# Kernel optimization log

Hardware: AMD Instinct MI355X
Metric: run time of the kernel (lower is better)

Reference implementation:

```python
import jax, jax.numpy as jnp
import numpy as np

N_SRC = 200000
N_DST = 50000
N_EDGES = 800000
IN_FEATS = 128
OUT_FEATS = 64


def setup_inputs() -> dict:
    key = jax.random.key(0)
    k1, k2, k3, k4 = jax.random.split(key, 4)
    x = jax.random.normal(k1, (N_SRC, IN_FEATS), dtype=jnp.float32)
    edge_src = jax.random.randint(k2, (N_EDGES,), 0, N_SRC, dtype=jnp.int64)
    edge_dst = jax.random.randint(k3, (N_EDGES,), 0, N_DST, dtype=jnp.int64)
    W = jax.random.normal(k4, (IN_FEATS, OUT_FEATS), dtype=jnp.float32) / np.sqrt(IN_FEATS)
    b = jnp.zeros((OUT_FEATS,), dtype=jnp.float32)
    return {"x": x, "edge_src": edge_src, "edge_dst": edge_dst, "W": W, "b": b, "n_dst": N_DST}


def reference(x, edge_src, edge_dst, W, b, n_dst):
    # DGL SAGEConv, aggregator_type='gcn'.
    # lin_before_mp = in_feats > out_feats (128 > 64) -> project before aggregation.
    h_src = x @ W                      # [n_src, out]
    h_dst = h_src[:n_dst]              # dst nodes are the first n_dst src nodes
    # sparse gather + segment reduce (SpMM): sum of projected neighbor feats per dst
    msgs = h_src[edge_src]             # [n_edges, out]
    neigh_sum = jax.ops.segment_sum(msgs, edge_dst, num_segments=n_dst)
    deg = jax.ops.segment_sum(jnp.ones_like(edge_dst, dtype=h_src.dtype),
                              edge_dst, num_segments=n_dst)  # in-degree per dst
    h = (neigh_sum + h_dst) / (deg + 1.0)[:, None]
    return h + b
```

## Files before the change

### kernel.cpp

```cpp
#include <hip/hip_runtime.h>
#include <hip/hip_bf16.h>

#define IN_F   128
#define OUT_F  64
#define NG 768
#define NB 256
#define CAP 64

typedef __attribute__((ext_vector_type(8))) short short8;
typedef __attribute__((ext_vector_type(4))) float floatx4;

__device__ inline unsigned short f32_to_bf16_rne(float f) {
    unsigned int u = __float_as_uint(f);
    unsigned int r = (u + 0x7FFFu + ((u >> 16) & 1u)) >> 16;
    return (unsigned short)r;
}
__device__ inline float bf16_to_f32(unsigned short u) {
    return __uint_as_float((unsigned int)u << 16);
}
__device__ inline unsigned int cvt_pk_bf16(float lo, float hi) {
    unsigned int r;
    asm volatile("v_cvt_pk_bf16_f32 %0, %1, %2" : "=v"(r) : "v"(lo), "v"(hi));
    return r;
}

__global__ __launch_bounds__(256) void prep_w(const float* __restrict__ W,
                                              unsigned short* __restrict__ Wtg) {
    const int o = blockIdx.x * 256 + threadIdx.x;
    #pragma unroll
    for (int m = 0; m < 4; ++m) {
        const int idx = o + m * 2048;
        const int f = idx >> 9, r = idx & 511, l = r >> 3, j = r & 7;
        const int t = f >> 2, s = f & 3;
        const int k = 32 * s + 8 * (l >> 4) + j;
        const int c = 16 * t + (l & 15);
        Wtg[idx] = f32_to_bf16_rne(W[k * 64 + c]);
    }
}

__global__ __launch_bounds__(256, 1) void gemm_bin(const float* __restrict__ x,
                                                   const unsigned short* __restrict__ Wtg,
                                                   unsigned short* __restrict__ h,
                                                   int nTiles,
                                                   const int* __restrict__ esrc,
                                                   const int* __restrict__ edst,
                                                   int* __restrict__ cnt,
                                                   int* __restrict__ elist,
                                                   int n_edges) {
    const int tid = threadIdx.x;

    if (blockIdx.x >= NG) {
        const int stride = NB * 256;
        for (int e = (blockIdx.x - NG) * 256 + tid; e < n_edges; e += stride) {
            const int d = edst[e];
            const int slot = atomicAdd(&cnt[d], 1);
            if (slot < CAP) elist[(size_t)d * CAP + slot] = esrc[e];
        }
        return;
    }

    const int lane = tid & 63;
    const int wave = tid >> 6;
    const int lrow = lane & 15;
    const int lkg  = lane >> 4;

    short8 bf[4][4];
    #pragma unroll
    for (int t = 0; t < 4; ++t)
        #pragma unroll
        for (int s = 0; s < 4; ++s)
            bf[t][s] = *reinterpret_cast<const short8*>(&Wtg[((t * 4 + s) * 64 + lane) * 8]);

    for (int tile = blockIdx.x; tile < nTiles; tile += NG) {
        const float* base = x + (size_t)tile * 64 * IN_F
                              + (size_t)(16 * wave + lrow) * IN_F + 8 * lkg;
        float4 x0 = *reinterpret_cast<const float4*>(base);
        float4 x1 = *reinterpret_cast<const float4*>(base + 4);
        float4 x2 = *reinterpret_cast<const float4*>(base + 32);
        float4 x3 = *reinterpret_cast<const float4*>(base + 36);
        float4 x4 = *reinterpret_cast<const float4*>(base + 64);
        float4 x5 = *reinterpret_cast<const float4*>(base + 68);
        float4 x6 = *reinterpret_cast<const float4*>(base + 96);
        float4 x7 = *reinterpret_cast<const float4*>(base + 100);

        short8 a0, a1, a2, a3;
        {
            union { unsigned int u[4]; short8 v; } cv;
            cv.u[0] = cvt_pk_bf16(x0.x, x0.y); cv.u[1] = cvt_pk_bf16(x0.z, x0.w);
            cv.u[2] = cvt_pk_bf16(x1.x, x1.y); cv.u[3] = cvt_pk_bf16(x1.z, x1.w);
            a0 = cv.v;
            cv.u[0] = cvt_pk_bf16(x2.x, x2.y); cv.u[1] = cvt_pk_bf16(x2.z, x2.w);
            cv.u[2] = cvt_pk_bf16(x3.x, x3.y); cv.u[3] = cvt_pk_bf16(x3.z, x3.w);
            a1 = cv.v;
            cv.u[0] = cvt_pk_bf16(x4.x, x4.y); cv.u[1] = cvt_pk_bf16(x4.z, x4.w);
            cv.u[2] = cvt_pk_bf16(x5.x, x5.y); cv.u[3] = cvt_pk_bf16(x5.z, x5.w);
            a2 = cv.v;
            cv.u[0] = cvt_pk_bf16(x6.x, x6.y); cv.u[1] = cvt_pk_bf16(x6.z, x6.w);
            cv.u[2] = cvt_pk_bf16(x7.x, x7.y); cv.u[3] = cvt_pk_bf16(x7.z, x7.w);
            a3 = cv.v;
        }

        floatx4 acc[4];
        #pragma unroll
        for (int t = 0; t < 4; ++t) acc[t] = (floatx4){0.f, 0.f, 0.f, 0.f};
        #pragma unroll
        for (int t = 0; t < 4; ++t) {
            acc[t] = __builtin_amdgcn_mfma_f32_16x16x32_bf16(a0, bf[t][0], acc[t], 0, 0, 0);
            acc[t] = __builtin_amdgcn_mfma_f32_16x16x32_bf16(a1, bf[t][1], acc[t], 0, 0, 0);
            acc[t] = __builtin_amdgcn_mfma_f32_16x16x32_bf16(a2, bf[t][2], acc[t], 0, 0, 0);
            acc[t] = __builtin_amdgcn_mfma_f32_16x16x32_bf16(a3, bf[t][3], acc[t], 0, 0, 0);
        }

        unsigned short* hb = h + ((size_t)tile * 64 + 16 * wave) * OUT_F;
        #pragma unroll
        for (int t = 0; t < 4; ++t)
            #pragma unroll
            for (int r = 0; r < 4; ++r)
                hb[(size_t)(4 * lkg + r) * OUT_F + 16 * t + lrow] =
                    f32_to_bf16_rne(acc[t][r]);
    }
}

__global__ __launch_bounds__(256) void gather_finalize(const unsigned short* __restrict__ h,
                                                       const int* __restrict__ cnt,
                                                       const int* __restrict__ elist,
                                                       const float* __restrict__ b,
                                                       float* __restrict__ out,
                                                       int n_dst) {
    const int lane = threadIdx.x & 63;
    const int d = blockIdx.x * 4 + (threadIdx.x >> 6);
    if (d >= n_dst) return;

    const int eq = lane >> 4;
    const int p  = lane & 15;

    const int cnt_d = cnt[d];
    const int m = min(cnt_d, CAP);
    const size_t ebase = (size_t)d * CAP;

    float4 acc = {0.f, 0.f, 0.f, 0.f};

    for (int base = 0; base < m; base += 64) {
        const int lim = min(64, m - base);
        const int sidx = (base + lane < m) ? elist[ebase + base + lane] : 0;
        for (int j = 0; j < lim; j += 4) {
            const int myj = j + eq;
            const bool valid = myj < lim;
            const int s = __shfl(sidx, valid ? myj : 0);
            const ushort4 v = *reinterpret_cast<const ushort4*>(&h[(size_t)s * OUT_F + 4 * p]);
            const float w = valid ? 1.0f : 0.0f;
            acc.x += w * bf16_to_f32(v.x);
            acc.y += w * bf16_to_f32(v.y);
            acc.z += w * bf16_to_f32(v.z);
            acc.w += w * bf16_to_f32(v.w);
        }
    }

    acc.x += __shfl_xor(acc.x, 32); acc.y += __shfl_xor(acc.y, 32);
    acc.z += __shfl_xor(acc.z, 32); acc.w += __shfl_xor(acc.w, 32);
    acc.x += __shfl_xor(acc.x, 16); acc.y += __shfl_xor(acc.y, 16);
    acc.z += __shfl_xor(acc.z, 16); acc.w += __shfl_xor(acc.w, 16);

    if (lane < 16) {
        const ushort4 hd = *reinterpret_cast<const ushort4*>(&h[(size_t)d * OUT_F + 4 * p]);
        const float4 bb = *reinterpret_cast<const float4*>(&b[4 * p]);
        const float inv = 1.0f / ((float)cnt_d + 1.0f);
        float4 o;
        o.x = (acc.x + bf16_to_f32(hd.x)) * inv + bb.x;
        o.y = (acc.y + bf16_to_f32(hd.y)) * inv + bb.y;
        o.z = (acc.z + bf16_to_f32(hd.z)) * inv + bb.z;
        o.w = (acc.w + bf16_to_f32(hd.w)) * inv + bb.w;
        *reinterpret_cast<float4*>(&out[(size_t)d * OUT_F + 4 * p]) = o;
    }
}

static inline size_t align256(size_t v) { return (v + 255) & ~(size_t)255; }

extern "C" void kernel_launch(void* const* d_in, const int* in_sizes, int n_in,
                              void* d_out, int out_size, void* d_ws, size_t ws_size,
                              hipStream_t stream) {
    const float* x    = (const float*)d_in[0];
    const int*   esrc = (const int*)d_in[1];
    const int*   edst = (const int*)d_in[2];
    const float* W    = (const float*)d_in[3];
    const float* b    = (const float*)d_in[4];

    const int n_rows  = in_sizes[0] / IN_F;
    const int n_edges = in_sizes[1];
    const int n_dst   = out_size / OUT_F;
    float* out = (float*)d_out;

    const size_t hBytes  = (size_t)n_rows * OUT_F * sizeof(unsigned short);
    const size_t cntOff  = align256(hBytes);
    const size_t elOff   = align256(cntOff + (size_t)n_dst * 4);
    const size_t wtOff   = align256(elOff + (size_t)n_dst * CAP * 4);
    const size_t needed  = wtOff + (size_t)IN_F * OUT_F * sizeof(unsigned short);

    unsigned short* h = (unsigned short*)d_ws;

    if (ws_size >= needed) {
        int* cnt             = (int*)((char*)d_ws + cntOff);
        int* elist           = (int*)((char*)d_ws + elOff);
        unsigned short* Wtg  = (unsigned short*)((char*)d_ws + wtOff);

        hipMemsetAsync(cnt, 0, (size_t)n_dst * 4, stream);

        prep_w<<<8, 256, 0, stream>>>(W, Wtg);

        const int nTiles = n_rows / 64;
        gemm_bin<<<NG + NB, 256, 0, stream>>>(x, Wtg, h, nTiles,
                                              esrc, edst, cnt, elist, n_edges);

        const int gBlocks = (n_dst + 3) / 4;
        gather_finalize<<<gBlocks, 256, 0, stream>>>(h, cnt, elist, b, out, n_dst);
    } else {
        hipMemsetAsync(out, 0, (size_t)out_size * sizeof(float), stream);
    }
}
```

Before: 95.94 us.

## Split edge binning into XCD-partitioned kernel with 16-bit dst indices

Edge binning moves out of the fused GEMM kernel into a separate kernel. Each block reads its XCD id from a hardware register and only handles destinations in that XCD's range, so atomics on cnt stay within one XCD's L2. A new prep kernel packs edge_dst into 16-bit values to cut the bytes each XCD rescans, and every XCD pulls edge chunks through its own atomic cursor. In exchange, each XCD now reads the whole dst array, there are extra kernel launches, and the GEMM no longer overlaps with binning. The 16-bit packing only holds while n_dst is below 65536.

```diff
diff --git a/kernel.cpp b/kernel.cpp
--- a/kernel.cpp
+++ b/kernel.cpp
@@ -3,12 +3,14 @@
 
 #define IN_F   128
 #define OUT_F  64
-#define NG 768
-#define NB 256
-#define CAP 64
+#define CAP    64
+#define NG     1024
+#define NBIN   2048
+#define CHUNK  2048
 
 typedef __attribute__((ext_vector_type(8))) short short8;
 typedef __attribute__((ext_vector_type(4))) float floatx4;
+typedef __attribute__((ext_vector_type(8))) unsigned short ushort8;
 
 __device__ inline unsigned short f32_to_bf16_rne(float f) {
     unsigned int u = __float_as_uint(f);
@@ -24,41 +26,81 @@
     return r;
 }
 
-__global__ __launch_bounds__(256) void prep_w(const float* __restrict__ W,
-                                              unsigned short* __restrict__ Wtg) {
-    const int o = blockIdx.x * 256 + threadIdx.x;
-    #pragma unroll
-    for (int m = 0; m < 4; ++m) {
-        const int idx = o + m * 2048;
-        const int f = idx >> 9, r = idx & 511, l = r >> 3, j = r & 7;
-        const int t = f >> 2, s = f & 3;
-        const int k = 32 * s + 8 * (l >> 4) + j;
-        const int c = 16 * t + (l & 15);
-        Wtg[idx] = f32_to_bf16_rne(W[k * 64 + c]);
-    }
-}
-
-__global__ __launch_bounds__(256, 1) void gemm_bin(const float* __restrict__ x,
-                                                   const unsigned short* __restrict__ Wtg,
-                                                   unsigned short* __restrict__ h,
-                                                   int nTiles,
-                                                   const int* __restrict__ esrc,
-                                                   const int* __restrict__ edst,
-                                                   int* __restrict__ cnt,
-                                                   int* __restrict__ elist,
-                                                   int n_edges) {
+__global__ __launch_bounds__(256) void prep(const float* __restrict__ W,
+                                            unsigned short* __restrict__ Wtg,
+                                            const int* __restrict__ edst,
+                                            unsigned short* __restrict__ edst16,
+                                            int n_edges) {
     const int tid = threadIdx.x;
-
-    if (blockIdx.x >= NG) {
-        const int stride = NB * 256;
-        for (int e = (blockIdx.x - NG) * 256 + tid; e < n_edges; e += stride) {
-            const int d = edst[e];
-            const int slot = atomicAdd(&cnt[d], 1);
-            if (slot < CAP) elist[(size_t)d * CAP + slot] = esrc[e];
+    if (blockIdx.x < 8) {
+        const int o = blockIdx.x * 256 + tid;
+        #pragma unroll
+        for (int m = 0; m < 4; ++m) {
+            const int idx = o + m * 2048;
+            const int f = idx >> 9, r = idx & 511, l = r >> 3, j = r & 7;
+            const int t = f >> 2, s = f & 3;
+            const int k = 32 * s + 8 * (l >> 4) + j;
+            const int c = 16 * t + (l & 15);
+            Wtg[idx] = f32_to_bf16_rne(W[k * 64 + c]);
         }
         return;
     }
-
+    const int e = ((blockIdx.x - 8) * 256 + tid) * 4;
+    if (e + 3 < n_edges) {
+        const int4 d4 = *reinterpret_cast<const int4*>(&edst[e]);
+        ushort4 o4;
+        o4.x = (unsigned short)d4.x; o4.y = (unsigned short)d4.y;
+        o4.z = (unsigned short)d4.z; o4.w = (unsigned short)d4.w;
+        *reinterpret_cast<ushort4*>(&edst16[e]) = o4;
+    } else {
+        for (int j = 0; j < 4 && e + j < n_edges; ++j)
+            edst16[e + j] = (unsigned short)edst[e + j];
+    }
+}
+
+__global__ __launch_bounds__(256) void bin_xcd(const unsigned short* __restrict__ edst16,
+                                               const int* __restrict__ esrc,
+                                               int* __restrict__ cursor,
+                                               int* __restrict__ cnt,
+                                               int* __restrict__ elist,
+                                               int n_dst, int n_edges) {
+    __shared__ int e0_s;
+    const int xcd = __builtin_amdgcn_s_getreg((3 << 11) | (0 << 6) | 20) & 7;
+    const int drange = (n_dst + 7) >> 3;
+    const int dlo = xcd * drange;
+    const int dhi = min(dlo + drange, n_dst);
+    const int tid = threadIdx.x;
+
+    for (;;) {
+        __syncthreads();
+        if (tid == 0) e0_s = atomicAdd(&cursor[xcd], CHUNK);
+        __syncthreads();
+        const int e0 = e0_s;
+        if (e0 >= n_edges) break;
+        const int nvec = min(CHUNK, n_edges - e0) >> 3;
+        if (tid < nvec) {
+            const int vidx = (e0 >> 3) + tid;
+            const ushort8 d8 = __builtin_nontemporal_load(
+                reinterpret_cast<const ushort8*>(edst16) + vidx);
+            const int ebase = vidx << 3;
+            #pragma unroll
+            for (int j = 0; j < 8; ++j) {
+                const int d = (int)d8[j];
+                if (d >= dlo && d < dhi) {
+                    const int s = esrc[ebase + j];
+                    const int slot = atomicAdd(&cnt[d], 1);
+                    if (slot < CAP) elist[(size_t)d * CAP + slot] = s;
+                }
+            }
+        }
+    }
+}
+
+__global__ __launch_bounds__(256, 1) void gemm_xw(const float* __restrict__ x,
+                                                  const unsigned short* __restrict__ Wtg,
+                                                  unsigned short* __restrict__ h,
+                                                  int nTiles) {
+    const int tid = threadIdx.x;
     const int lane = tid & 63;
     const int wave = tid >> 6;
     const int lrow = lane & 15;
@@ -192,24 +234,31 @@
 
     const size_t hBytes  = (size_t)n_rows * OUT_F * sizeof(unsigned short);
     const size_t cntOff  = align256(hBytes);
-    const size_t elOff   = align256(cntOff + (size_t)n_dst * 4);
-    const size_t wtOff   = align256(elOff + (size_t)n_dst * CAP * 4);
+    const size_t curOff  = cntOff + (size_t)n_dst * 4;
+    const size_t elOff   = align256(curOff + 8 * 4);
+    const size_t e16Off  = align256(elOff + (size_t)n_dst * CAP * 4);
+    const size_t wtOff   = align256(e16Off + (size_t)n_edges * sizeof(unsigned short));
     const size_t needed  = wtOff + (size_t)IN_F * OUT_F * sizeof(unsigned short);
 
     unsigned short* h = (unsigned short*)d_ws;
 
     if (ws_size >= needed) {
-        int* cnt             = (int*)((char*)d_ws + cntOff);
-        int* elist           = (int*)((char*)d_ws + elOff);
-        unsigned short* Wtg  = (unsigned short*)((char*)d_ws + wtOff);
-
-        hipMemsetAsync(cnt, 0, (size_t)n_dst * 4, stream);
-
-        prep_w<<<8, 256, 0, stream>>>(W, Wtg);
+        int* cnt               = (int*)((char*)d_ws + cntOff);
+        int* cursor            = (int*)((char*)d_ws + curOff);
+        int* elist             = (int*)((char*)d_ws + elOff);
+        unsigned short* edst16 = (unsigned short*)((char*)d_ws + e16Off);
+        unsigned short* Wtg    = (unsigned short*)((char*)d_ws + wtOff);
+
+        hipMemsetAsync(cnt, 0, (size_t)n_dst * 4 + 8 * 4, stream);
+
+        const int pBlocks = 8 + (n_edges + 1023) / 1024;
+        prep<<<pBlocks, 256, 0, stream>>>(W, Wtg, edst, edst16, n_edges);
+
+        bin_xcd<<<NBIN, 256, 0, stream>>>(edst16, esrc, cursor, cnt, elist,
+                                          n_dst, n_edges);
 
         const int nTiles = n_rows / 64;
-        gemm_bin<<<NG + NB, 256, 0, stream>>>(x, Wtg, h, nTiles,
-                                              esrc, edst, cnt, elist, n_edges);
+        gemm_xw<<<NG, 256, 0, stream>>>(x, Wtg, h, nTiles);
 
         const int gBlocks = (n_dst + 3) / 4;
         gather_finalize<<<gBlocks, 256, 0, stream>>>(h, cnt, elist, b, out, n_dst);
```

Measured after the change: 143.6 us. 49.7% more time.
